# Kernel optimization log

Hardware: AMD Instinct MI355X
Metric: run time of the kernel (lower is better)

## Reference

```python
import jax, jax.numpy as jnp
import numpy as np

TAU = 2.0
EPS = 1e-5
T, B, C, H, W = 4, 16, 256, 32, 32
HEADS = 8
HD = C // HEADS
N = H * W


def make_spike(grad_fn):
    @jax.custom_vjp
    def f(x):
        return (x >= 0.0).astype(x.dtype)
    def fwd(x):
        return f(x), x
    def bwd(res, g):
        return (g * grad_fn(res),)
    f.defvjp(fwd, bwd)
    return f

# ATan surrogate (alpha=5.0) used by q/k/v LIF nodes
spike_atan5 = make_spike(lambda x: (5.0 / 2.0) / (1.0 + (jnp.pi / 2.0 * 5.0 * x) ** 2))
# default Sigmoid surrogate (alpha=4.0) for shortcut_lif / talking_heads_lif
def _sig_grad(x):
    s = jax.nn.sigmoid(4.0 * x)
    return 4.0 * s * (1.0 - s)
spike_sig4 = make_spike(_sig_grad)


def lif(x, spike, v_th=1.0):
    # multi-step LIF over leading time axis; hard reset to 0, detach_reset
    def step(v, xt):
        h = v + (xt - v) / TAU
        s = spike(h - v_th)
        v_new = h * (1.0 - jax.lax.stop_gradient(s))
        return v_new, s
    _, out = jax.lax.scan(step, jnp.zeros_like(x[0]), x)
    return out


def conv1x1(x, w):
    # x: (T,B,C,H,W), w: (Cout,Cin) from Conv2d kernel_size=1
    return jnp.einsum('tbchw,oc->tbohw', x, w)


def bn(y, gamma, beta, mean, var):
    scale = (gamma / jnp.sqrt(var + EPS))[None, None, :, None, None]
    shift = (beta - mean * gamma / jnp.sqrt(var + EPS))[None, None, :, None, None]
    return y * scale + shift


def to_heads(x):
    # (T,B,C,H,W) -> (T,B,heads,N,hd); matches flatten(3).transpose(-1,-2).reshape.permute
    x = x.reshape(T, B, C, N).transpose(0, 1, 3, 2)          # (T,B,N,C)
    x = x.reshape(T, B, N, HEADS, HD).transpose(0, 1, 3, 2, 4)  # (T,B,heads,N,hd)
    return x


def setup_inputs() -> dict:
    key = jax.random.key(0)
    ks = jax.random.split(key, 20)
    def bn_params(i):
        return (1.0 + 0.1 * jax.random.normal(ks[i], (C,), jnp.float32),
                0.1 * jax.random.normal(ks[i + 1], (C,), jnp.float32),
                0.1 * jax.random.normal(ks[i + 2], (C,), jnp.float32),
                jax.random.uniform(ks[i + 3], (C,), jnp.float32, 0.5, 1.5))
    q_g, q_b, q_m, q_var = bn_params(1)
    k_g, k_b, k_m, k_var = bn_params(5)
    v_g, v_b, v_m, v_var = bn_params(9)
    p_g, p_b, p_m, p_var = bn_params(13)
    std = 1.0 / np.sqrt(C)
    return {
        'x': jax.random.normal(ks[0], (T, B, C, H, W), jnp.float32),
        'q_w': std * jax.random.normal(ks[17], (C, C), jnp.float32),
        'q_g': q_g, 'q_b': q_b, 'q_m': q_m, 'q_var': q_var,
        'k_w': std * jax.random.normal(ks[18], (C, C), jnp.float32),
        'k_g': k_g, 'k_b': k_b, 'k_m': k_m, 'k_var': k_var,
        'v_w': std * jax.random.normal(ks[19], (C, C), jnp.float32),
        'v_g': v_g, 'v_b': v_b, 'v_m': v_m, 'v_var': v_var,
        'proj_w': std * jax.random.normal(ks[4], (C, C), jnp.float32),
        'proj_bias': 0.01 * jax.random.normal(ks[8], (C,), jnp.float32),
        'p_g': p_g, 'p_b': p_b, 'p_m': p_m, 'p_var': p_var,
    }


def reference(x, q_w, q_g, q_b, q_m, q_var, k_w, k_g, k_b, k_m, k_var,
              v_w, v_g, v_b, v_m, v_var, proj_w, proj_bias, p_g, p_b, p_m, p_var):
    identity = x
    xs = lif(x, spike_sig4, 1.0)                      # shortcut_lif
    q = to_heads(lif(bn(conv1x1(xs, q_w), q_g, q_b, q_m, q_var), spike_atan5, 1.0))
    k = to_heads(lif(bn(conv1x1(xs, k_w), k_g, k_b, k_m, k_var), spike_atan5, 1.0))
    v = to_heads(lif(bn(conv1x1(xs, v_w), v_g, v_b, v_m, v_var), spike_atan5, 1.0))
    kv = jnp.sum(k * v, axis=-2, keepdims=True)       # (T,B,heads,1,hd)
    kv = lif(kv, spike_sig4, 0.5)                     # talking_heads_lif, v_th=0.5
    attn = q * kv                                     # (T,B,heads,N,hd)
    # transpose(3,4).reshape(T,B,C,H,W)
    out = attn.transpose(0, 1, 2, 4, 3).reshape(T, B, C, H, W)
    out = conv1x1(out, proj_w) + proj_bias[None, None, :, None, None]
    out = bn(out, p_g, p_b, p_m, p_var)
    out = out + identity
    return out, v
```

## Files before the change

### kernel.cpp

```cpp
#include <hip/hip_runtime.h>
#include <hip/hip_bf16.h>
#include <stdint.h>

#define T_ 4
#define B_ 16
#define C_ 256
#define N_ 1024
#define HEADS_ 8
#define HD_ 32

typedef unsigned long long u64;
typedef unsigned char u8;

__global__ __launch_bounds__(256) void prep_transpose(
    const float* __restrict__ qw, const float* __restrict__ kw,
    const float* __restrict__ vw, const float* __restrict__ pw,
    float* __restrict__ wtq, float* __restrict__ wtk,
    float* __restrict__ wtv, float* __restrict__ wtp) {
  int c = blockIdx.x;
  int o = threadIdx.x;
  wtq[c * C_ + o] = qw[o * C_ + c];
  wtk[c * C_ + o] = kw[o * C_ + c];
  wtv[c * C_ + o] = vw[o * C_ + c];
  wtp[c * C_ + o] = pw[o * C_ + c];
}

__global__ __launch_bounds__(256) void prep_bn(
    const float* __restrict__ qg, const float* __restrict__ qb2,
    const float* __restrict__ qmn, const float* __restrict__ qvr,
    const float* __restrict__ kg, const float* __restrict__ kb2,
    const float* __restrict__ kmn, const float* __restrict__ kvr,
    const float* __restrict__ vg, const float* __restrict__ vb2,
    const float* __restrict__ vmn, const float* __restrict__ vvr,
    const float* __restrict__ pg, const float* __restrict__ pb2,
    const float* __restrict__ pmn, const float* __restrict__ pvr,
    float* __restrict__ bnt) {
  int c = threadIdx.x;
  float rs;
  rs = sqrtf(qvr[c] + 1e-5f);
  bnt[0 * C_ + c] = qg[c] / rs;
  bnt[1 * C_ + c] = qb2[c] - qmn[c] * qg[c] / rs;
  rs = sqrtf(kvr[c] + 1e-5f);
  bnt[2 * C_ + c] = kg[c] / rs;
  bnt[3 * C_ + c] = kb2[c] - kmn[c] * kg[c] / rs;
  rs = sqrtf(vvr[c] + 1e-5f);
  bnt[4 * C_ + c] = vg[c] / rs;
  bnt[5 * C_ + c] = vb2[c] - vmn[c] * vg[c] / rs;
  rs = sqrtf(pvr[c] + 1e-5f);
  bnt[6 * C_ + c] = pg[c] / rs;
  bnt[7 * C_ + c] = pb2[c] - pmn[c] * pg[c] / rs;
}

__global__ __launch_bounds__(256) void lif_shortcut(const float* __restrict__ x,
                                                    u64* __restrict__ xsm) {
  int b = blockIdx.x >> 5;
  int n0 = (blockIdx.x & 31) << 5;
  int tid = threadIdx.x;
  int l = tid & 63, w = tid >> 6;
  __shared__ float tile[C_ * 33];
  float v[32];
#pragma unroll
  for (int i = 0; i < 32; i++) v[i] = 0.f;
  int c = (w << 6) + l;
  for (int t = 0; t < T_; t++) {
    __syncthreads();
    const float* xp = x + (((size_t)t * B_ + b) * C_) * N_ + n0;
    for (int idx = tid; idx < C_ * 32; idx += 256) {
      int cc = idx >> 5, nn = idx & 31;
      tile[cc * 33 + nn] = xp[(size_t)cc * N_ + nn];
    }
    __syncthreads();
#pragma unroll
    for (int nn = 0; nn < 32; nn++) {
      float xv = tile[c * 33 + nn];
      float h = v[nn] + (xv - v[nn]) * 0.5f;
      bool s = h >= 1.0f;
      v[nn] = s ? 0.f : h;
      u64 bal = __ballot(s);
      if (l == nn) xsm[(((size_t)t * B_ + b) * N_ + n0 + nn) * 4 + w] = bal;
    }
  }
}

__global__ __launch_bounds__(256) void qkv_sparse(
    const u64* __restrict__ xsm,
    const float* __restrict__ wtq, const float* __restrict__ wtk,
    const float* __restrict__ wtv, const float* __restrict__ bnt,
    float* __restrict__ pkv, u64* __restrict__ qm_out,
    float* __restrict__ vout) {
  int b = blockIdx.x >> 7;
  int nt = blockIdx.x & 127;
  int n0 = nt << 3;
  int tid = threadIdx.x;
  int l = tid & 63, wv = tid >> 6;
  float qs[4], qsh[4], ks[4], ksh[4], vsc[4], vsh[4];
#pragma unroll
  for (int j = 0; j < 4; j++) {
    int o = (j << 6) + l;
    qs[j]  = bnt[0 * C_ + o]; qsh[j] = bnt[1 * C_ + o];
    ks[j]  = bnt[2 * C_ + o]; ksh[j] = bnt[3 * C_ + o];
    vsc[j] = bnt[4 * C_ + o]; vsh[j] = bnt[5 * C_ + o];
  }
  int cnt[4][4];
#pragma unroll
  for (int t = 0; t < 4; t++)
#pragma unroll
    for (int j = 0; j < 4; j++) cnt[t][j] = 0;

  for (int nn = wv; nn < 8; nn += 4) {
    int n = n0 + nn;
    float aq[4][4], ak[4][4], av[4][4];
#pragma unroll
    for (int t = 0; t < 4; t++)
#pragma unroll
      for (int j = 0; j < 4; j++) { aq[t][j] = 0.f; ak[t][j] = 0.f; av[t][j] = 0.f; }
#pragma unroll
    for (int t = 0; t < 4; t++) {
      const u64* mp = xsm + ((((size_t)t * B_ + b) * N_ + n) << 2);
#pragma unroll
      for (int wd = 0; wd < 4; wd++) {
        u64 m = mp[wd];
        while (m) {
          int c = (wd << 6) + __builtin_ctzll(m);
          m &= (m - 1);
          const float* rq = wtq + c * C_;
          const float* rk = wtk + c * C_;
          const float* rv = wtv + c * C_;
#pragma unroll
          for (int j = 0; j < 4; j++) {
            int o = (j << 6) + l;
            aq[t][j] += rq[o];
            ak[t][j] += rk[o];
            av[t][j] += rv[o];
          }
        }
      }
    }
#pragma unroll
    for (int j = 0; j < 4; j++) {
      int o = (j << 6) + l;
      float vq = 0.f, vk = 0.f, vv = 0.f;
#pragma unroll
      for (int t = 0; t < 4; t++) {
        float pq = aq[t][j] * qs[j] + qsh[j];
        float pk = ak[t][j] * ks[j] + ksh[j];
        float pv = av[t][j] * vsc[j] + vsh[j];
        float hq = vq + (pq - vq) * 0.5f;
        float hk = vk + (pk - vk) * 0.5f;
        float hv = vv + (pv - vv) * 0.5f;
        bool sq = hq >= 1.0f; vq = sq ? 0.f : hq;
        bool sk = hk >= 1.0f; vk = sk ? 0.f : hk;
        bool sv = hv >= 1.0f; vv = sv ? 0.f : hv;
        cnt[t][j] += (sk && sv) ? 1 : 0;
        vout[(((size_t)t * B_ + b) * HEADS_ + (o >> 5)) * ((size_t)N_ * HD_) +
             (size_t)n * HD_ + (o & 31)] = sv ? 1.0f : 0.0f;
        u64 bal = __ballot(sq);
        if (l == (t << 2) + j)
          qm_out[((((size_t)t * B_ + b) * N_ + n) << 2) + j] = bal;
      }
    }
  }
  __shared__ int scnt[4][4][C_];
#pragma unroll
  for (int t = 0; t < 4; t++)
#pragma unroll
    for (int j = 0; j < 4; j++) scnt[wv][t][(j << 6) + l] = cnt[t][j];
  __syncthreads();
  for (int idx = tid; idx < 4 * C_; idx += 256) {
    int t = idx >> 8, c = idx & 255;
    int s = scnt[0][t][c] + scnt[1][t][c] + scnt[2][t][c] + scnt[3][t][c];
    pkv[(((size_t)t * B_ + b) * 128 + nt) * C_ + c] = (float)s;
  }
}

__global__ __launch_bounds__(256) void kv_lif_kernel(const float* __restrict__ pkv,
                                                     u64* __restrict__ kvsm) {
  int b = blockIdx.x;
  int c = threadIdx.x;
  int l = c & 63, j = c >> 6;
  float v = 0.f;
  for (int t = 0; t < 4; t++) {
    const float* p = pkv + (((size_t)t * B_ + b) * 128) * C_ + c;
    float kv = 0.f;
#pragma unroll
    for (int i = 0; i < 128; i++) kv += p[(size_t)i * C_];
    float h = v + (kv - v) * 0.5f;
    bool s = h >= 0.5f;
    v = s ? 0.f : h;
    u64 bal = __ballot(s);
    if (l == t) kvsm[((size_t)t * B_ + b) * 4 + j] = bal;
  }
}

__global__ __launch_bounds__(256) void proj_sparse(
    const u64* __restrict__ qm, const u64* __restrict__ kvsm,
    const float* __restrict__ wtp, const float* __restrict__ bnt,
    const float* __restrict__ pbias, const float* __restrict__ x,
    float* __restrict__ out) {
  int tb = blockIdx.x >> 5;
  int n0 = (blockIdx.x & 31) << 5;
  int t = tb >> 4, b = tb & 15;
  int tid = threadIdx.x;
  int l = tid & 63, w = tid >> 6;
  __shared__ float tile[C_ * 33];
  u64 kvm[4];
#pragma unroll
  for (int wd = 0; wd < 4; wd++) kvm[wd] = kvsm[((size_t)t * B_ + b) * 4 + wd];
  for (int nn = w; nn < 32; nn += 4) {
    int n = n0 + nn;
    float acc[4] = {0.f, 0.f, 0.f, 0.f};
    const u64* mp = qm + ((((size_t)t * B_ + b) * N_ + n) << 2);
#pragma unroll
    for (int wd = 0; wd < 4; wd++) {
      u64 m = mp[wd] & kvm[wd];
      while (m) {
        int c = (wd << 6) + __builtin_ctzll(m);
        m &= (m - 1);
        const float* rp = wtp + c * C_;
#pragma unroll
        for (int j = 0; j < 4; j++) acc[j] += rp[(j << 6) + l];
      }
    }
#pragma unroll
    for (int j = 0; j < 4; j++) tile[((j << 6) + l) * 33 + nn] = acc[j];
  }
  __syncthreads();
  int col = l & 31;
  int half = l >> 5;
  for (int r = (w << 1) + half; r < C_; r += 8) {
    float val = tile[r * 33 + col];
    float z = (val + pbias[r]) * bnt[6 * C_ + r] + bnt[7 * C_ + r];
    size_t xi = (((size_t)t * B_ + b) * C_ + r) * N_ + n0 + col;
    out[xi] = z + x[xi];
  }
}

__global__ __launch_bounds__(256) void fill_zero_f32(float* p, size_t n) {
  size_t i = (size_t)blockIdx.x * 256 + threadIdx.x;
  if (i < n) p[i] = 0.0f;
}

extern "C" void kernel_launch(void* const* d_in, const int* in_sizes, int n_in,
                              void* d_out, int out_size, void* d_ws, size_t ws_size,
                              hipStream_t stream) {
  const float* x  = (const float*)d_in[0];
  const float* qw = (const float*)d_in[1];
  const float* qg = (const float*)d_in[2];
  const float* qb = (const float*)d_in[3];
  const float* qm = (const float*)d_in[4];
  const float* qv = (const float*)d_in[5];
  const float* kw = (const float*)d_in[6];
  const float* kg = (const float*)d_in[7];
  const float* kb = (const float*)d_in[8];
  const float* km = (const float*)d_in[9];
  const float* kv = (const float*)d_in[10];
  const float* vw = (const float*)d_in[11];
  const float* vg = (const float*)d_in[12];
  const float* vb2 = (const float*)d_in[13];
  const float* vm = (const float*)d_in[14];
  const float* vv = (const float*)d_in[15];
  const float* pw = (const float*)d_in[16];
  const float* pbias = (const float*)d_in[17];
  const float* pg = (const float*)d_in[18];
  const float* pb = (const float*)d_in[19];
  const float* pm = (const float*)d_in[20];
  const float* pv = (const float*)d_in[21];

  const size_t needed = 13641728ull;
  if (ws_size < needed) {
    size_t n = (size_t)out_size;
    fill_zero_f32<<<(unsigned)((n + 255) / 256), 256, 0, stream>>>(
        (float*)d_out, n);
    return;
  }

  char* ws = (char*)d_ws;
  float* wtq = (float*)(ws + 0);
  float* wtk = (float*)(ws + 262144);
  float* wtv = (float*)(ws + 524288);
  float* wtp = (float*)(ws + 786432);
  float* bnt = (float*)(ws + 1048576);
  u64*   xsm = (u64*)  (ws + 1056768);
  u64*   qmm = (u64*)  (ws + 3153920);
  float* pkv = (float*)(ws + 5251072);
  u64*   kvsm = (u64*) (ws + 13639680);

  float* out  = (float*)d_out;
  float* vout = out + (size_t)T_ * B_ * C_ * N_;

  prep_transpose<<<256, 256, 0, stream>>>(qw, kw, vw, pw, wtq, wtk, wtv, wtp);
  prep_bn<<<1, 256, 0, stream>>>(qg, qb, qm, qv, kg, kb, km, kv,
                                 vg, vb2, vm, vv, pg, pb, pm, pv, bnt);
  lif_shortcut<<<512, 256, 0, stream>>>(x, xsm);
  qkv_sparse<<<2048, 256, 0, stream>>>(xsm, wtq, wtk, wtv, bnt, pkv, qmm, vout);
  kv_lif_kernel<<<16, 256, 0, stream>>>(pkv, kvsm);
  proj_sparse<<<2048, 256, 0, stream>>>(qmm, kvsm, wtp, bnt, pbias, x, out);
}
```

Baseline: 146.9 us.

## Stage QKV weight slabs in LDS and process 32 positions per block

The sparse QKV kernel is restructured so each block handles 32 spatial positions instead of 8. The q, k and v weights are streamed through shared memory in 64-row slabs, and the spike-mask walk reads from LDS four rows at a time rather than gathering rows from global memory. The q, k and v passes now run one after another, with the k spikes kept as ballots in shared memory for the kv count. This cuts global weight traffic and the partial-count buffer, in exchange for about 66KB of LDS per block, more barriers, and only 512 blocks.

```diff
diff --git a/kernel.cpp b/kernel.cpp
--- a/kernel.cpp
+++ b/kernel.cpp
@@ -82,94 +82,189 @@
   }
 }
 
-__global__ __launch_bounds__(256) void qkv_sparse(
+__device__ __forceinline__ void pass_walk(const float* __restrict__ wt,
+                                          float* __restrict__ buf,
+                                          const u64 (*msks)[4][4],
+                                          float acc[8][4][4],
+                                          int tid, int l, int wv) {
+#pragma unroll
+  for (int s = 0; s < 8; s++)
+#pragma unroll
+    for (int t = 0; t < 4; t++)
+#pragma unroll
+      for (int j = 0; j < 4; j++) acc[s][t][j] = 0.f;
+  for (int wd = 0; wd < 4; wd++) {
+    __syncthreads();
+#pragma unroll
+    for (int i = 0; i < 16; i++) {
+      int idx = (i << 8) + tid;
+      ((float4*)buf)[idx] = ((const float4*)(wt + ((size_t)wd << 14)))[idx];
+    }
+    __syncthreads();
+#pragma unroll
+    for (int s = 0; s < 8; s++) {
+      int ls = (wv << 3) + s;
+#pragma unroll
+      for (int t = 0; t < 4; t++) {
+        u64 m = msks[ls][t][wd];
+        while (m) {
+          int c0 = __builtin_ctzll(m); m &= m - 1;
+          int c1 = 64, c2 = 64, c3 = 64;
+          if (m) { c1 = __builtin_ctzll(m); m &= m - 1; }
+          if (m) { c2 = __builtin_ctzll(m); m &= m - 1; }
+          if (m) { c3 = __builtin_ctzll(m); m &= m - 1; }
+          const float* p0 = buf + (c0 << 8) + l;
+          const float* p1 = buf + (c1 << 8) + l;
+          const float* p2 = buf + (c2 << 8) + l;
+          const float* p3 = buf + (c3 << 8) + l;
+          float r00 = p0[0], r01 = p0[64], r02 = p0[128], r03 = p0[192];
+          float r10 = p1[0], r11 = p1[64], r12 = p1[128], r13 = p1[192];
+          float r20 = p2[0], r21 = p2[64], r22 = p2[128], r23 = p2[192];
+          float r30 = p3[0], r31 = p3[64], r32 = p3[128], r33 = p3[192];
+          acc[s][t][0] += r00; acc[s][t][0] += r10;
+          acc[s][t][0] += r20; acc[s][t][0] += r30;
+          acc[s][t][1] += r01; acc[s][t][1] += r11;
+          acc[s][t][1] += r21; acc[s][t][1] += r31;
+          acc[s][t][2] += r02; acc[s][t][2] += r12;
+          acc[s][t][2] += r22; acc[s][t][2] += r32;
+          acc[s][t][3] += r03; acc[s][t][3] += r13;
+          acc[s][t][3] += r23; acc[s][t][3] += r33;
+        }
+      }
+    }
+  }
+}
+
+__global__ __launch_bounds__(256, 2) void qkv_lds(
     const u64* __restrict__ xsm,
     const float* __restrict__ wtq, const float* __restrict__ wtk,
     const float* __restrict__ wtv, const float* __restrict__ bnt,
     float* __restrict__ pkv, u64* __restrict__ qm_out,
     float* __restrict__ vout) {
-  int b = blockIdx.x >> 7;
-  int nt = blockIdx.x & 127;
-  int n0 = nt << 3;
+  int b = blockIdx.x >> 5;
+  int nt = blockIdx.x & 31;
+  int n0 = nt << 5;
   int tid = threadIdx.x;
   int l = tid & 63, wv = tid >> 6;
-  float qs[4], qsh[4], ks[4], ksh[4], vsc[4], vsh[4];
-#pragma unroll
-  for (int j = 0; j < 4; j++) {
-    int o = (j << 6) + l;
-    qs[j]  = bnt[0 * C_ + o]; qsh[j] = bnt[1 * C_ + o];
-    ks[j]  = bnt[2 * C_ + o]; ksh[j] = bnt[3 * C_ + o];
-    vsc[j] = bnt[4 * C_ + o]; vsh[j] = bnt[5 * C_ + o];
-  }
+
+  __shared__ float buf[65 * 256];
+  __shared__ u64 msks[32][4][4];
+  __shared__ u64 kball[32][4][4];
+
+  buf[64 * 256 + tid] = 0.f;
+#pragma unroll
+  for (int r = 0; r < 2; r++) {
+    int idx = (r << 8) + tid;
+    int ls = idx >> 4, t = (idx >> 2) & 3, wd = idx & 3;
+    msks[ls][t][wd] =
+        xsm[((((size_t)t * B_ + b) * N_ + n0 + ls) << 2) + wd];
+  }
+
+  float acc[8][4][4];
+
+  pass_walk(wtq, buf, msks, acc, tid, l, wv);
+  {
+    float sc[4], sh[4];
+#pragma unroll
+    for (int j = 0; j < 4; j++) {
+      sc[j] = bnt[0 * C_ + (j << 6) + l];
+      sh[j] = bnt[1 * C_ + (j << 6) + l];
+    }
+#pragma unroll
+    for (int s = 0; s < 8; s++) {
+      int n = n0 + (wv << 3) + s;
+#pragma unroll
+      for (int j = 0; j < 4; j++) {
+        float vq = 0.f;
+#pragma unroll
+        for (int t = 0; t < 4; t++) {
+          float p = acc[s][t][j] * sc[j] + sh[j];
+          float h = vq + (p - vq) * 0.5f;
+          bool sq = h >= 1.0f;
+          vq = sq ? 0.f : h;
+          u64 bq = __ballot(sq);
+          if (l == (t << 2) + j)
+            qm_out[((((size_t)t * B_ + b) * N_ + n) << 2) + j] = bq;
+        }
+      }
+    }
+  }
+
+  pass_walk(wtk, buf, msks, acc, tid, l, wv);
+  {
+    float sc[4], sh[4];
+#pragma unroll
+    for (int j = 0; j < 4; j++) {
+      sc[j] = bnt[2 * C_ + (j << 6) + l];
+      sh[j] = bnt[3 * C_ + (j << 6) + l];
+    }
+#pragma unroll
+    for (int s = 0; s < 8; s++) {
+      int ls = (wv << 3) + s;
+#pragma unroll
+      for (int j = 0; j < 4; j++) {
+        float vk = 0.f;
+#pragma unroll
+        for (int t = 0; t < 4; t++) {
+          float p = acc[s][t][j] * sc[j] + sh[j];
+          float h = vk + (p - vk) * 0.5f;
+          bool sk = h >= 1.0f;
+          vk = sk ? 0.f : h;
+          u64 bk = __ballot(sk);
+          if (l == (t << 2) + j) kball[ls][t][j] = bk;
+        }
+      }
+    }
+  }
+
+  pass_walk(wtv, buf, msks, acc, tid, l, wv);
   int cnt[4][4];
 #pragma unroll
   for (int t = 0; t < 4; t++)
 #pragma unroll
     for (int j = 0; j < 4; j++) cnt[t][j] = 0;
-
-  for (int nn = wv; nn < 8; nn += 4) {
-    int n = n0 + nn;
-    float aq[4][4], ak[4][4], av[4][4];
-#pragma unroll
-    for (int t = 0; t < 4; t++)
-#pragma unroll
-      for (int j = 0; j < 4; j++) { aq[t][j] = 0.f; ak[t][j] = 0.f; av[t][j] = 0.f; }
-#pragma unroll
-    for (int t = 0; t < 4; t++) {
-      const u64* mp = xsm + ((((size_t)t * B_ + b) * N_ + n) << 2);
-#pragma unroll
-      for (int wd = 0; wd < 4; wd++) {
-        u64 m = mp[wd];
-        while (m) {
-          int c = (wd << 6) + __builtin_ctzll(m);
-          m &= (m - 1);
-          const float* rq = wtq + c * C_;
-          const float* rk = wtk + c * C_;
-          const float* rv = wtv + c * C_;
-#pragma unroll
-          for (int j = 0; j < 4; j++) {
-            int o = (j << 6) + l;
-            aq[t][j] += rq[o];
-            ak[t][j] += rk[o];
-            av[t][j] += rv[o];
-          }
+  {
+    float sc[4], sh[4];
+#pragma unroll
+    for (int j = 0; j < 4; j++) {
+      sc[j] = bnt[4 * C_ + (j << 6) + l];
+      sh[j] = bnt[5 * C_ + (j << 6) + l];
+    }
+#pragma unroll
+    for (int s = 0; s < 8; s++) {
+      int ls = (wv << 3) + s;
+      int n = n0 + ls;
+#pragma unroll
+      for (int j = 0; j < 4; j++) {
+        int o = (j << 6) + l;
+        float vv = 0.f;
+#pragma unroll
+        for (int t = 0; t < 4; t++) {
+          float p = acc[s][t][j] * sc[j] + sh[j];
+          float h = vv + (p - vv) * 0.5f;
+          bool sv = h >= 1.0f;
+          vv = sv ? 0.f : h;
+          vout[(((size_t)t * B_ + b) * HEADS_ + (o >> 5)) * ((size_t)N_ * HD_) +
+               (size_t)n * HD_ + (o & 31)] = sv ? 1.0f : 0.0f;
+          cnt[t][j] += (((kball[ls][t][j] >> l) & 1ull) && sv) ? 1 : 0;
         }
       }
     }
-#pragma unroll
-    for (int j = 0; j < 4; j++) {
-      int o = (j << 6) + l;
-      float vq = 0.f, vk = 0.f, vv = 0.f;
-#pragma unroll
-      for (int t = 0; t < 4; t++) {
-        float pq = aq[t][j] * qs[j] + qsh[j];
-        float pk = ak[t][j] * ks[j] + ksh[j];
-        float pv = av[t][j] * vsc[j] + vsh[j];
-        float hq = vq + (pq - vq) * 0.5f;
-        float hk = vk + (pk - vk) * 0.5f;
-        float hv = vv + (pv - vv) * 0.5f;
-        bool sq = hq >= 1.0f; vq = sq ? 0.f : hq;
-        bool sk = hk >= 1.0f; vk = sk ? 0.f : hk;
-        bool sv = hv >= 1.0f; vv = sv ? 0.f : hv;
-        cnt[t][j] += (sk && sv) ? 1 : 0;
-        vout[(((size_t)t * B_ + b) * HEADS_ + (o >> 5)) * ((size_t)N_ * HD_) +
-             (size_t)n * HD_ + (o & 31)] = sv ? 1.0f : 0.0f;
-        u64 bal = __ballot(sq);
-        if (l == (t << 2) + j)
-          qm_out[((((size_t)t * B_ + b) * N_ + n) << 2) + j] = bal;
-      }
-    }
-  }
-  __shared__ int scnt[4][4][C_];
+  }
+
+  __syncthreads();
+  int* scnt = (int*)buf;
 #pragma unroll
   for (int t = 0; t < 4; t++)
 #pragma unroll
-    for (int j = 0; j < 4; j++) scnt[wv][t][(j << 6) + l] = cnt[t][j];
+    for (int j = 0; j < 4; j++)
+      scnt[((wv << 2) + t) * C_ + (j << 6) + l] = cnt[t][j];
   __syncthreads();
   for (int idx = tid; idx < 4 * C_; idx += 256) {
     int t = idx >> 8, c = idx & 255;
-    int s = scnt[0][t][c] + scnt[1][t][c] + scnt[2][t][c] + scnt[3][t][c];
-    pkv[(((size_t)t * B_ + b) * 128 + nt) * C_ + c] = (float)s;
+    int s = scnt[(0 + t) * C_ + c] + scnt[(4 + t) * C_ + c] +
+            scnt[(8 + t) * C_ + c] + scnt[(12 + t) * C_ + c];
+    pkv[(((size_t)t * B_ + b) * 32 + nt) * C_ + c] = (float)s;
   }
 }
 
@@ -180,10 +275,10 @@
   int l = c & 63, j = c >> 6;
   float v = 0.f;
   for (int t = 0; t < 4; t++) {
-    const float* p = pkv + (((size_t)t * B_ + b) * 128) * C_ + c;
+    const float* p = pkv + (((size_t)t * B_ + b) * 32) * C_ + c;
     float kv = 0.f;
 #pragma unroll
-    for (int i = 0; i < 128; i++) kv += p[(size_t)i * C_];
+    for (int i = 0; i < 32; i++) kv += p[(size_t)i * C_];
     float h = v + (kv - v) * 0.5f;
     bool s = h >= 0.5f;
     v = s ? 0.f : h;
@@ -266,7 +361,7 @@
   const float* pm = (const float*)d_in[20];
   const float* pv = (const float*)d_in[21];
 
-  const size_t needed = 13641728ull;
+  const size_t needed = 7350272ull;
   if (ws_size < needed) {
     size_t n = (size_t)out_size;
     fill_zero_f32<<<(unsigned)((n + 255) / 256), 256, 0, stream>>>(
@@ -283,7 +378,7 @@
   u64*   xsm = (u64*)  (ws + 1056768);
   u64*   qmm = (u64*)  (ws + 3153920);
   float* pkv = (float*)(ws + 5251072);
-  u64*   kvsm = (u64*) (ws + 13639680);
+  u64*   kvsm = (u64*) (ws + 7348224);
 
   float* out  = (float*)d_out;
   float* vout = out + (size_t)T_ * B_ * C_ * N_;
@@ -292,7 +387,7 @@
   prep_bn<<<1, 256, 0, stream>>>(qg, qb, qm, qv, kg, kb, km, kv,
                                  vg, vb2, vm, vv, pg, pb, pm, pv, bnt);
   lif_shortcut<<<512, 256, 0, stream>>>(x, xsm);
-  qkv_sparse<<<2048, 256, 0, stream>>>(xsm, wtq, wtk, wtv, bnt, pkv, qmm, vout);
+  qkv_lds<<<512, 256, 0, stream>>>(xsm, wtq, wtk, wtv, bnt, pkv, qmm, vout);
   kv_lif_kernel<<<16, 256, 0, stream>>>(pkv, kvsm);
   proj_sparse<<<2048, 256, 0, stream>>>(qmm, kvsm, wtp, bnt, pbias, x, out);
 }
```

Measured after the change: 204.6 us. 1.39x slower.
